# Optimization experiments

Measured on AMD Instinct MI355X. Metric: run time of the kernel, lower is better.

## Reference

```python
import jax, jax.numpy as jnp
import numpy as np

# ANI symmetry-function hyperparameters (module defaults)
RCR = 5.2
RCA = 3.5
ETAR = 16.0
ETAA = 8.0
ZETA = 32.0
NSPEC = 8  # len(elements) * 2 for dimer_aev
SHFR = jnp.linspace(0.9, RCR - (RCR - 0.9) / 16.0, 16)   # [16]
SHFA = jnp.linspace(0.9, RCA - (RCA - 0.9) / 4.0, 4)     # [4]
SHFZ = jnp.linspace(np.pi / 16.0, np.pi - np.pi / 16.0, 8)  # [8]
_TRIU_I, _TRIU_J = np.triu_indices(NSPEC)                 # 36 unordered species pairs
_PAIR_SCALE = jnp.asarray(np.where(_TRIU_I == _TRIU_J, 0.5, 1.0), dtype=jnp.float32)


def _cutoff(d, rc):
    # TorchANI cosine cutoff: 0.5*cos(pi*d/rc)+0.5 inside rc, 0 outside
    return jnp.where(d <= rc, 0.5 * jnp.cos(np.pi * d / rc) + 0.5, 0.0)


def _compute_aev(species_wb, coords):
    # species_wb: [B,A] int in [0,8); coords: [B,A,3]
    B, A = species_wb.shape
    diff = coords[:, None, :, :] - coords[:, :, None, :]   # [B,A,A,3] vec i->j
    d2 = jnp.sum(diff * diff, axis=-1)                     # [B,A,A]
    dist = jnp.sqrt(jnp.where(d2 > 0, d2, 1.0))            # safe sqrt (diag masked below)
    valid = ~jnp.eye(A, dtype=bool)[None]                  # [1,A,A] exclude self pairs
    oh = jax.nn.one_hot(species_wb, NSPEC, dtype=coords.dtype)  # [B,A,8]

    # ---- radial AEV ----
    fcr = _cutoff(dist, RCR) * valid                       # [B,A,A]
    rterm = 0.25 * jnp.exp(-ETAR * (dist[..., None] - SHFR) ** 2) * fcr[..., None]  # [B,A,A,16]
    radial = jnp.einsum('bijr,bjs->bisr', rterm, oh).reshape(B, A, NSPEC * 16)      # [B,A,128]

    # ---- angular AEV ----
    fca = _cutoff(dist, RCA) * valid                       # [B,A,A]
    unit = diff / dist[..., None]                          # [B,A,A,3]
    cos_t = jnp.einsum('bijd,bikd->bijk', unit, unit)      # [B,A,A,A]
    theta = jnp.arccos(0.95 * jnp.clip(cos_t, -1.0, 1.0))  # TorchANI 0.95 stabilizer
    f1 = ((1.0 + jnp.cos(theta[..., None] - SHFZ)) * 0.5) ** ZETA        # [B,A,A,A,8]
    ravg = 0.5 * (dist[:, :, :, None] + dist[:, :, None, :])             # [B,A,A,A]
    f2 = jnp.exp(-ETAA * (ravg[..., None] - SHFA) ** 2)                  # [B,A,A,A,4]
    jk_neq = ~jnp.eye(A, dtype=bool)[None, None]                          # exclude j==k
    w = (fca[:, :, :, None] * fca[:, :, None, :]) * jk_neq               # [B,A,A,A]
    g2 = 2.0 * f2 * w[..., None]                                          # [B,A,A,A,4]
    # scatter ordered (j,k) neighbor pairs onto species-pair grid
    M = jnp.einsum('bijkz,bijka,bjs,bkt->bistaz', f1, g2, oh, oh)        # [B,A,8,8,4,8]
    ang = M[:, :, _TRIU_I, _TRIU_J] * _PAIR_SCALE[None, None, :, None, None]  # [B,A,36,4,8]
    return jnp.concatenate([radial, ang.reshape(B, A, 36 * 4 * 8)], axis=-1)   # [B,A,1280]


def _mlp(x, W1, b1, W2, b2, W3, b3, W4, b4):
    h = jax.nn.celu(x @ W1 + b1, alpha=0.1)
    h = jax.nn.celu(h @ W2 + b2, alpha=0.1)
    h = jax.nn.celu(h @ W3 + b3, alpha=0.1)
    return h @ W4 + b4


def setup_inputs() -> dict:
    key = jax.random.key(0)
    ks = jax.random.split(key, 8)
    B, A = 32, 32
    species = jax.random.randint(ks[0], (B, A), 0, 4)          # elements H,C,N,O
    coordinates = jax.random.uniform(ks[1], (B, A, 3), dtype=jnp.float32) * 9.0  # 9 A box
    belongings = jax.random.randint(ks[2], (B, A), 1, 3)       # monomer id in {1,2}
    approx = jax.random.normal(ks[3], (B, A), dtype=jnp.float32)
    dims = [1281, 64, 32, 16, 1]
    params = {}
    for i in range(4):
        std = float(np.sqrt(2.0 / (dims[i] + dims[i + 1])))  # xavier normal
        params['W%d' % (i + 1)] = jax.random.normal(ks[4 + i % 4], (dims[i], dims[i + 1]), dtype=jnp.float32) * std
        params['b%d' % (i + 1)] = jnp.zeros((dims[i + 1],), dtype=jnp.float32)
    return dict(species=species, coordinates=coordinates, belongings=belongings, approx=approx, **params)


def reference(species, coordinates, belongings, approx, W1, b1, W2, b2, W3, b3, W4, b4):
    # dimer_aev path: shift species by monomer membership (num_species=4)
    species_wb = species + (belongings - 1) * 4
    aev = _compute_aev(species_wb, coordinates)                      # [B,A,1280]
    aev = jnp.concatenate([aev, approx[..., None].astype(aev.dtype)], axis=-1)  # [B,A,1281]
    per_atom = _mlp(aev, W1, b1, W2, b2, W3, b3, W4, b4)             # [B,A,1]
    return per_atom.sum(axis=1)                                      # [B,1]
```

## Files before the change

kernel.cpp:

```cpp
#include <hip/hip_runtime.h>
#include <math.h>


#define NB 32
#define NA 32
#define FLAG_MAGIC 0x3C96A5F1

__device__ __forceinline__ float celu01(float x) {
    return x > 0.0f ? x : 0.1f * expm1f(x * 10.0f);
}

__global__ __launch_bounds__(1024)
void fused_kernel(const int* __restrict__ species, const float* __restrict__ coords,
                  const int* __restrict__ belong, const float* __restrict__ approx,
                  const float* __restrict__ W1, const float* __restrict__ b1,
                  const float* __restrict__ W2, const float* __restrict__ b2,
                  const float* __restrict__ W3, const float* __restrict__ b3,
                  const float* __restrict__ W4, const float* __restrict__ b4,
                  float* __restrict__ partial, int* __restrict__ flags,
                  float* __restrict__ out) {
    const int blk = blockIdx.x;
    const int b = blk >> 3, grp = blk & 7;
    const int t = threadIdx.x;
    const float PI = 3.14159265358979323846f;

    __shared__ float cx[32], cy[32], cz[32];
    __shared__ int   spec[32];
    __shared__ float dists[4][32], fcas[4][32], uxs[4][32], uys[4][32], uzs[4][32];
    __shared__ int   nbr[4][32];
    __shared__ int   cnt[4];
    __shared__ __align__(16) float aev[4][1284];
    __shared__ float part[16][4][64];
    __shared__ float h1[4][64], h2[4][32], h3[4][16];
    __shared__ float czl[8], szl[8];
    __shared__ float evals[4];
    __shared__ float peers[8];

    if (t < 32) {
        int g = b * NA + t;
        cx[t] = coords[g*3+0]; cy[t] = coords[g*3+1]; cz[t] = coords[g*3+2];
        spec[t] = species[g] + (belong[g]-1)*4;
    }
    if (t < 8) {
        float th = PI/16.0f + (float)t * (PI/8.0f);
        czl[t] = cosf(th); szl[t] = sinf(th);
    }
    for (int idx = t; idx < 4*1284; idx += 1024) ((float*)aev)[idx] = 0.0f;
    __syncthreads();

    if (t < 128) {
        const int li = t >> 5, j = t & 31;
        const int ia = grp*4 + li;
        float dx = cx[j]-cx[ia], dy = cy[j]-cy[ia], dz = cz[j]-cz[ia];
        float d2 = dx*dx + dy*dy + dz*dz;
        float d = sqrtf(d2 > 0.0f ? d2 : 1.0f);
        float inv = 1.0f / d;
        dists[li][j] = d;
        uxs[li][j] = dx*inv; uys[li][j] = dy*inv; uzs[li][j] = dz*inv;
        bool self = (j == ia);
        float fca = (!self && d <= 3.5f) ? (0.5f*cosf(PI*d/3.5f)+0.5f) : 0.0f;
        fcas[li][j] = fca;

        if (!self && d <= 5.2f) {
            float f = 0.5f*cosf(PI*d/5.2f) + 0.5f;
            int base = spec[j]*16;
            #pragma unroll
            for (int r = 0; r < 16; ++r) {
                float dd = d - (0.9f + 0.26875f*(float)r);
                atomicAdd(&aev[li][base+r], 0.25f*expf(-16.0f*dd*dd)*f);
            }
        }
        bool act = (fca > 0.0f);
        unsigned long long mask = __ballot(act);
        unsigned int half = (t & 32) ? (unsigned int)(mask >> 32)
                                     : (unsigned int)(mask & 0xFFFFFFFFull);
        int l31 = t & 31;
        int pos = __popc(half & ((1u << l31) - 1u));
        if (act) nbr[li][pos] = j;
        if (l31 == 0) cnt[li] = __popc(half);
    }
    __syncthreads();

    {
        const int li = t >> 8, lane = t & 255;
        const int n2 = cnt[li];
        const int npairs = n2*(n2-1)/2;
        for (int p = lane; p < npairs; p += 256) {
            int m = 0, rem = p, rl = n2 - 1;
            while (rem >= rl) { rem -= rl; --rl; ++m; }
            int n = m + 1 + rem;
            int j = nbr[li][m], k = nbr[li][n];

            float wjk = fcas[li][j] * fcas[li][k];
            float cd = uxs[li][j]*uxs[li][k] + uys[li][j]*uys[li][k] + uzs[li][j]*uzs[li][k];
            cd = fminf(fmaxf(cd, -1.0f), 1.0f);
            float cth = 0.95f * cd;
            float sth = sqrtf(1.0f - cth*cth);
            float ravg = 0.5f * (dists[li][j] + dists[li][k]);

            float f1[8];
            #pragma unroll
            for (int z = 0; z < 8; ++z) {
                float base = 0.5f*(1.0f + cth*czl[z] + sth*szl[z]);
                float x2 = base*base; x2 = x2*x2; x2 = x2*x2; x2 = x2*x2; x2 = x2*x2;
                f1[z] = x2;
            }
            int sj = spec[j], sk = spec[k];
            int smin = sj < sk ? sj : sk, smax = sj < sk ? sk : sj;
            int pp = 8*smin - (smin*(smin-1))/2 + (smax - smin);
            float w2 = 2.0f * wjk;
            #pragma unroll
            for (int a = 0; a < 4; ++a) {
                float da = ravg - (0.9f + 0.65f*(float)a);
                float f2 = expf(-8.0f*da*da) * w2;
                int bb = 128 + pp*32 + a*8;
                #pragma unroll
                for (int z = 0; z < 8; ++z) atomicAdd(&aev[li][bb+z], f2*f1[z]);
            }
        }
    }
    if (t < 4) aev[t][1280] = approx[b*NA + grp*4 + t];
    __syncthreads();

    {
        const int c = t & 63, q = t >> 6;
        float a0 = 0.0f, a1 = 0.0f, a2 = 0.0f, a3 = 0.0f;
        const float4* x0 = (const float4*)(&aev[0][0]);
        const float4* x1 = (const float4*)(&aev[1][0]);
        const float4* x2 = (const float4*)(&aev[2][0]);
        const float4* x3 = (const float4*)(&aev[3][0]);
        const int r4beg = q * 20;
        #pragma unroll 4
        for (int rr = 0; rr < 20; ++rr) {
            const int r4 = r4beg + rr;
            const int rb = r4 * 4;
            float w1a = W1[(rb+0)*64 + c];
            float w1b = W1[(rb+1)*64 + c];
            float w1c = W1[(rb+2)*64 + c];
            float w1d = W1[(rb+3)*64 + c];
            float4 v0 = x0[r4], v1 = x1[r4], v2 = x2[r4], v3 = x3[r4];
            a0 = fmaf(v0.x, w1a, a0); a0 = fmaf(v0.y, w1b, a0);
            a0 = fmaf(v0.z, w1c, a0); a0 = fmaf(v0.w, w1d, a0);
            a1 = fmaf(v1.x, w1a, a1); a1 = fmaf(v1.y, w1b, a1);
            a1 = fmaf(v1.z, w1c, a1); a1 = fmaf(v1.w, w1d, a1);
            a2 = fmaf(v2.x, w1a, a2); a2 = fmaf(v2.y, w1b, a2);
            a2 = fmaf(v2.z, w1c, a2); a2 = fmaf(v2.w, w1d, a2);
            a3 = fmaf(v3.x, w1a, a3); a3 = fmaf(v3.y, w1b, a3);
            a3 = fmaf(v3.z, w1c, a3); a3 = fmaf(v3.w, w1d, a3);
        }
        part[q][0][c] = a0; part[q][1][c] = a1;
        part[q][2][c] = a2; part[q][3][c] = a3;
    }
    __syncthreads();
    if (t < 256) {
        const int c = t & 63, w = t >> 6;
        float acc = b1[c] + aev[w][1280] * W1[1280*64 + c];
        #pragma unroll
        for (int q = 0; q < 16; q += 4)
            acc += ((part[q][w][c] + part[q+1][w][c]) + (part[q+2][w][c] + part[q+3][w][c]));
        h1[w][c] = celu01(acc);
    }
    __syncthreads();

    if (t < 128) {
        int a = t >> 5, cc = t & 31;
        float s = b2[cc];
        #pragma unroll 8
        for (int r = 0; r < 64; ++r) s = fmaf(h1[a][r], W2[r*32 + cc], s);
        h2[a][cc] = celu01(s);
    }
    __syncthreads();

    if (t < 64) {
        int a = t >> 4, cc = t & 15;
        float s = b3[cc];
        #pragma unroll
        for (int r = 0; r < 32; ++r) s = fmaf(h2[a][r], W3[r*16 + cc], s);
        h3[a][cc] = celu01(s);
    }
    __syncthreads();

    if (t < 4) {
        float e = b4[0];
        #pragma unroll
        for (int r = 0; r < 16; ++r) e = fmaf(h3[t][r], W4[r], e);
        evals[t] = e;
    }
    __syncthreads();

    if (grp != 0) {
        if (t == 0) {
            float v = (evals[0]+evals[1]) + (evals[2]+evals[3]);
            __hip_atomic_store(&partial[blk], v, __ATOMIC_RELAXED, __HIP_MEMORY_SCOPE_AGENT);
            __hip_atomic_store(&flags[blk], FLAG_MAGIC, __ATOMIC_RELEASE, __HIP_MEMORY_SCOPE_AGENT);
        }
    } else {
        if (t == 0) peers[0] = (evals[0]+evals[1]) + (evals[2]+evals[3]);
        if (t >= 1 && t < 8) {
            int src = blk + t;
            while (__hip_atomic_load(&flags[src], __ATOMIC_ACQUIRE,
                                     __HIP_MEMORY_SCOPE_AGENT) != FLAG_MAGIC) { }
            peers[t] = __hip_atomic_load(&partial[src], __ATOMIC_RELAXED,
                                         __HIP_MEMORY_SCOPE_AGENT);
            __hip_atomic_store(&flags[src], 0, __ATOMIC_RELAXED,
                               __HIP_MEMORY_SCOPE_AGENT);
        }
        __syncthreads();
        if (t == 0) {
            float s = ((peers[0]+peers[1]) + (peers[2]+peers[3]))
                    + ((peers[4]+peers[5]) + (peers[6]+peers[7]));
            out[b] = s;
        }
    }
}

extern "C" void kernel_launch(void* const* d_in, const int* in_sizes, int n_in,
                              void* d_out, int out_size, void* d_ws, size_t ws_size,
                              hipStream_t stream) {
    (void)in_sizes; (void)n_in; (void)ws_size; (void)out_size;
    const int*   species = (const int*)d_in[0];
    const float* coords  = (const float*)d_in[1];
    const int*   belong  = (const int*)d_in[2];
    const float* approx  = (const float*)d_in[3];
    const float* W1 = (const float*)d_in[4];  const float* b1 = (const float*)d_in[5];
    const float* W2 = (const float*)d_in[6];  const float* b2 = (const float*)d_in[7];
    const float* W3 = (const float*)d_in[8];  const float* b3 = (const float*)d_in[9];
    const float* W4 = (const float*)d_in[10]; const float* b4 = (const float*)d_in[11];
    float* partial = (float*)d_ws;
    int*   flags   = ((int*)d_ws) + 256;
    float* out     = (float*)d_out;

    fused_kernel<<<NB * 8, 1024, 0, stream>>>(species, coords, belong, approx,
                                              W1, b1, W2, b2, W3, b3, W4, b4,
                                              partial, flags, out);
}
```

Before: 23.77 us.

## Prefetch W1 rows into registers early and shrink angular stage to 256 threads

Threads 256-1023 now load the first 32 of their 80 W1 rows into registers at kernel start, so those global loads overlap the AEV computation. Only threads 0-255 do the angular pair work, with 64 lanes per atom, which leaves the other waves idle and able to hold the prefetched weights. The sin/cos table setup moves to threads 64-71. The cost is 32 extra live registers across the AEV phase and less parallelism for the angular pairs, which could hurt occupancy or angular throughput.

```diff
diff --git a/kernel.cpp b/kernel.cpp
--- a/kernel.cpp
+++ b/kernel.cpp
@@ -36,14 +36,33 @@
     __shared__ float evals[4];
     __shared__ float peers[8];
 
+    float w1h0=0,w1h1=0,w1h2=0,w1h3=0,w1h4=0,w1h5=0,w1h6=0,w1h7=0,
+          w1h8=0,w1h9=0,w1h10=0,w1h11=0,w1h12=0,w1h13=0,w1h14=0,w1h15=0,
+          w1h16=0,w1h17=0,w1h18=0,w1h19=0,w1h20=0,w1h21=0,w1h22=0,w1h23=0,
+          w1h24=0,w1h25=0,w1h26=0,w1h27=0,w1h28=0,w1h29=0,w1h30=0,w1h31=0;
+    if (t >= 256) {
+        const int c = t & 63, q = t >> 6;
+        const float* Wp = W1 + (size_t)(q * 80) * 64 + c;
+        w1h0  = Wp[ 0*64]; w1h1  = Wp[ 1*64]; w1h2  = Wp[ 2*64]; w1h3  = Wp[ 3*64];
+        w1h4  = Wp[ 4*64]; w1h5  = Wp[ 5*64]; w1h6  = Wp[ 6*64]; w1h7  = Wp[ 7*64];
+        w1h8  = Wp[ 8*64]; w1h9  = Wp[ 9*64]; w1h10 = Wp[10*64]; w1h11 = Wp[11*64];
+        w1h12 = Wp[12*64]; w1h13 = Wp[13*64]; w1h14 = Wp[14*64]; w1h15 = Wp[15*64];
+        w1h16 = Wp[16*64]; w1h17 = Wp[17*64]; w1h18 = Wp[18*64]; w1h19 = Wp[19*64];
+        w1h20 = Wp[20*64]; w1h21 = Wp[21*64]; w1h22 = Wp[22*64]; w1h23 = Wp[23*64];
+        w1h24 = Wp[24*64]; w1h25 = Wp[25*64]; w1h26 = Wp[26*64]; w1h27 = Wp[27*64];
+        w1h28 = Wp[28*64]; w1h29 = Wp[29*64]; w1h30 = Wp[30*64]; w1h31 = Wp[31*64];
+    }
+    __builtin_amdgcn_sched_barrier(0);
+
     if (t < 32) {
         int g = b * NA + t;
         cx[t] = coords[g*3+0]; cy[t] = coords[g*3+1]; cz[t] = coords[g*3+2];
         spec[t] = species[g] + (belong[g]-1)*4;
     }
-    if (t < 8) {
-        float th = PI/16.0f + (float)t * (PI/8.0f);
-        czl[t] = cosf(th); szl[t] = sinf(th);
+    if (t >= 64 && t < 72) {
+        int z = t - 64;
+        float th = PI/16.0f + (float)z * (PI/8.0f);
+        czl[z] = cosf(th); szl[z] = sinf(th);
     }
     for (int idx = t; idx < 4*1284; idx += 1024) ((float*)aev)[idx] = 0.0f;
     __syncthreads();
@@ -81,11 +100,11 @@
     }
     __syncthreads();
 
-    {
-        const int li = t >> 8, lane = t & 255;
+    if (t < 256) {
+        const int li = t >> 6, lane = t & 63;
         const int n2 = cnt[li];
         const int npairs = n2*(n2-1)/2;
-        for (int p = lane; p < npairs; p += 256) {
+        for (int p = lane; p < npairs; p += 64) {
             int m = 0, rem = p, rl = n2 - 1;
             while (rem >= rl) { rem -= rl; --rl; ++m; }
             int n = m + 1 + rem;
@@ -130,23 +149,65 @@
         const float4* x2 = (const float4*)(&aev[2][0]);
         const float4* x3 = (const float4*)(&aev[3][0]);
         const int r4beg = q * 20;
-        #pragma unroll 4
-        for (int rr = 0; rr < 20; ++rr) {
-            const int r4 = r4beg + rr;
-            const int rb = r4 * 4;
-            float w1a = W1[(rb+0)*64 + c];
-            float w1b = W1[(rb+1)*64 + c];
-            float w1c = W1[(rb+2)*64 + c];
-            float w1d = W1[(rb+3)*64 + c];
-            float4 v0 = x0[r4], v1 = x1[r4], v2 = x2[r4], v3 = x3[r4];
-            a0 = fmaf(v0.x, w1a, a0); a0 = fmaf(v0.y, w1b, a0);
-            a0 = fmaf(v0.z, w1c, a0); a0 = fmaf(v0.w, w1d, a0);
-            a1 = fmaf(v1.x, w1a, a1); a1 = fmaf(v1.y, w1b, a1);
-            a1 = fmaf(v1.z, w1c, a1); a1 = fmaf(v1.w, w1d, a1);
-            a2 = fmaf(v2.x, w1a, a2); a2 = fmaf(v2.y, w1b, a2);
-            a2 = fmaf(v2.z, w1c, a2); a2 = fmaf(v2.w, w1d, a2);
-            a3 = fmaf(v3.x, w1a, a3); a3 = fmaf(v3.y, w1b, a3);
-            a3 = fmaf(v3.z, w1c, a3); a3 = fmaf(v3.w, w1d, a3);
+
+        if (t >= 256) {
+            #define HELD_STEP(RR, WA, WB, WC, WD)                                  \
+            {   const int r4 = r4beg + RR;                                         \
+                float4 v0 = x0[r4], v1 = x1[r4], v2 = x2[r4], v3 = x3[r4];         \
+                a0 = fmaf(v0.x, WA, a0); a0 = fmaf(v0.y, WB, a0);                  \
+                a0 = fmaf(v0.z, WC, a0); a0 = fmaf(v0.w, WD, a0);                  \
+                a1 = fmaf(v1.x, WA, a1); a1 = fmaf(v1.y, WB, a1);                  \
+                a1 = fmaf(v1.z, WC, a1); a1 = fmaf(v1.w, WD, a1);                  \
+                a2 = fmaf(v2.x, WA, a2); a2 = fmaf(v2.y, WB, a2);                  \
+                a2 = fmaf(v2.z, WC, a2); a2 = fmaf(v2.w, WD, a2);                  \
+                a3 = fmaf(v3.x, WA, a3); a3 = fmaf(v3.y, WB, a3);                  \
+                a3 = fmaf(v3.z, WC, a3); a3 = fmaf(v3.w, WD, a3); }
+            HELD_STEP(0, w1h0,  w1h1,  w1h2,  w1h3)
+            HELD_STEP(1, w1h4,  w1h5,  w1h6,  w1h7)
+            HELD_STEP(2, w1h8,  w1h9,  w1h10, w1h11)
+            HELD_STEP(3, w1h12, w1h13, w1h14, w1h15)
+            HELD_STEP(4, w1h16, w1h17, w1h18, w1h19)
+            HELD_STEP(5, w1h20, w1h21, w1h22, w1h23)
+            HELD_STEP(6, w1h24, w1h25, w1h26, w1h27)
+            HELD_STEP(7, w1h28, w1h29, w1h30, w1h31)
+            #undef HELD_STEP
+            #pragma unroll 4
+            for (int rr = 8; rr < 20; ++rr) {
+                const int r4 = r4beg + rr;
+                const int rb = r4 * 4;
+                float w1a = W1[(rb+0)*64 + c];
+                float w1b = W1[(rb+1)*64 + c];
+                float w1c = W1[(rb+2)*64 + c];
+                float w1d = W1[(rb+3)*64 + c];
+                float4 v0 = x0[r4], v1 = x1[r4], v2 = x2[r4], v3 = x3[r4];
+                a0 = fmaf(v0.x, w1a, a0); a0 = fmaf(v0.y, w1b, a0);
+                a0 = fmaf(v0.z, w1c, a0); a0 = fmaf(v0.w, w1d, a0);
+                a1 = fmaf(v1.x, w1a, a1); a1 = fmaf(v1.y, w1b, a1);
+                a1 = fmaf(v1.z, w1c, a1); a1 = fmaf(v1.w, w1d, a1);
+                a2 = fmaf(v2.x, w1a, a2); a2 = fmaf(v2.y, w1b, a2);
+                a2 = fmaf(v2.z, w1c, a2); a2 = fmaf(v2.w, w1d, a2);
+                a3 = fmaf(v3.x, w1a, a3); a3 = fmaf(v3.y, w1b, a3);
+                a3 = fmaf(v3.z, w1c, a3); a3 = fmaf(v3.w, w1d, a3);
+            }
+        } else {
+            #pragma unroll 4
+            for (int rr = 0; rr < 20; ++rr) {
+                const int r4 = r4beg + rr;
+                const int rb = r4 * 4;
+                float w1a = W1[(rb+0)*64 + c];
+                float w1b = W1[(rb+1)*64 + c];
+                float w1c = W1[(rb+2)*64 + c];
+                float w1d = W1[(rb+3)*64 + c];
+                float4 v0 = x0[r4], v1 = x1[r4], v2 = x2[r4], v3 = x3[r4];
+                a0 = fmaf(v0.x, w1a, a0); a0 = fmaf(v0.y, w1b, a0);
+                a0 = fmaf(v0.z, w1c, a0); a0 = fmaf(v0.w, w1d, a0);
+                a1 = fmaf(v1.x, w1a, a1); a1 = fmaf(v1.y, w1b, a1);
+                a1 = fmaf(v1.z, w1c, a1); a1 = fmaf(v1.w, w1d, a1);
+                a2 = fmaf(v2.x, w1a, a2); a2 = fmaf(v2.y, w1b, a2);
+                a2 = fmaf(v2.z, w1c, a2); a2 = fmaf(v2.w, w1d, a2);
+                a3 = fmaf(v3.x, w1a, a3); a3 = fmaf(v3.y, w1b, a3);
+                a3 = fmaf(v3.z, w1c, a3); a3 = fmaf(v3.w, w1d, a3);
+            }
         }
         part[q][0][c] = a0; part[q][1][c] = a1;
         part[q][2][c] = a2; part[q][3][c] = a3;
```

After: 24.82 us. 4.4% more time.
